# Kernel optimization log

Hardware: AMD Instinct MI355X
Metric: run time of the kernel (lower is better)

## Reference

```python
import jax, jax.numpy as jnp
import numpy as np

EPS = 1e-06

def rotate_half(x):
    d = x.shape[-1] // 2
    return jnp.concatenate([-x[..., d:], x[..., :d]], axis=-1)

def rmsnorm(x, w):
    rms = jnp.sqrt(jnp.mean(x * x, axis=-1, keepdims=True) + EPS)
    return (x / rms) * w

def setup_inputs() -> dict:
    key = jax.random.key(0)
    ks = jax.random.split(key, 12)
    H, Hq, Hkv, Dh, S, C = 2048, 16, 8, 128, 1, 16384
    sc = 0.02
    return {
        "hidden_states": jax.random.normal(ks[0], (1, 1, S, H), jnp.float32),
        "cos": jax.random.uniform(ks[1], (1, 1, S, Dh), jnp.float32),
        "sin": jax.random.uniform(ks[2], (1, 1, S, Dh), jnp.float32),
        "attention_mask": jnp.zeros((1, 1, S, C + S), jnp.float32),
        "k_cache": jax.random.normal(ks[3], (Hkv, Dh, C), jnp.float32),
        "v_cache": jax.random.normal(ks[4], (Hkv, C, Dh), jnp.float32),
        "Wq": jax.random.normal(ks[5], (Hq, Dh, H), jnp.float32) * sc,
        "Wk": jax.random.normal(ks[6], (Hkv, Dh, H), jnp.float32) * sc,
        "Wv": jax.random.normal(ks[7], (Hkv, Dh, H), jnp.float32) * sc,
        "Wo": jax.random.normal(ks[8], (H, Hq * Dh), jnp.float32) * sc,
        "q_norm_w": jnp.ones((Dh,), jnp.float32),
        "k_norm_w": jnp.ones((Dh,), jnp.float32),
    }

def reference(hidden_states, cos, sin, attention_mask, k_cache, v_cache, Wq, Wk, Wv, Wo, q_norm_w, k_norm_w):
    S = hidden_states.shape[2]
    Hq, Dh = Wq.shape[0], Wq.shape[1]
    Hkv = Wk.shape[0]
    g = Hq // Hkv
    x = hidden_states.reshape(S, -1)                      # [S, H]
    # per-head 1x1 conv == per-head linear; batched as einsum
    q = rmsnorm(jnp.einsum('sh,qdh->qsd', x, Wq), q_norm_w)   # [Hq, S, Dh]
    k = rmsnorm(jnp.einsum('sh,kdh->ksd', x, Wk), k_norm_w)   # [Hkv, S, Dh]
    v = jnp.einsum('sh,kdh->ksd', x, Wv)                      # [Hkv, S, Dh]
    c = cos.reshape(S, Dh)
    s = sin.reshape(S, Dh)
    q = q * c + rotate_half(q) * s
    k_new = k * c + rotate_half(k) * s
    # KV cache concat: k stored transposed [Hkv, Dh, C]
    k_full = jnp.concatenate([k_cache, jnp.swapaxes(k_new, 1, 2)], axis=2)  # [Hkv, Dh, C+S]
    v_full = jnp.concatenate([v_cache, v], axis=1)                          # [Hkv, C+S, Dh]
    kf = jnp.repeat(k_full, g, axis=0)                    # GQA expand -> [Hq, Dh, C+S]
    vf = jnp.repeat(v_full, g, axis=0)                    # [Hq, C+S, Dh]
    scaling = Dh ** -0.5
    scores = jnp.einsum('qsd,qdc->qsc', q, kf) * scaling + attention_mask.reshape(1, S, -1)
    probs = jax.nn.softmax(scores, axis=-1)
    out = jnp.einsum('qsc,qcd->qsd', probs, vf)           # [Hq, S, Dh]
    out = jnp.transpose(out, (1, 0, 2)).reshape(S, Hq * Dh)  # head-major last dim
    attn = out @ Wo.T                                     # o_proj 1x1 conv
    return attn.reshape(1, 1, S, -1), k_new, v
```

## Files before the change

kernel.cpp:

```cpp
#include <hip/hip_runtime.h>
#include <math.h>
#include <stddef.h>

#define HQ   16
#define HKV  8
#define DH   128
#define HID  2048
#define CC   16384
#define NCH  128
#define CHUNK 128


__global__ void k_qkv(const float* __restrict__ x,
                      const float* __restrict__ Wq,
                      const float* __restrict__ Wk,
                      const float* __restrict__ Wv,
                      float* __restrict__ raw,
                      float* __restrict__ out){
  int wave = threadIdx.x >> 6, lane = threadIdx.x & 63;
  int e = blockIdx.x * 4 + wave;
  const float* W;
  if (e < 2048)      W = Wq + (size_t)e * HID;
  else if (e < 3072) W = Wk + (size_t)(e - 2048) * HID;
  else               W = Wv + (size_t)(e - 3072) * HID;
  float4 wb[8], xb[8];
  #pragma unroll
  for (int j = 0; j < 8; ++j) wb[j] = *(const float4*)(W + (j * 64 + lane) * 4);
  #pragma unroll
  for (int j = 0; j < 8; ++j) xb[j] = *(const float4*)(x + (j * 64 + lane) * 4);
  float acc = 0.f;
  #pragma unroll
  for (int j = 0; j < 8; ++j)
    acc += wb[j].x*xb[j].x + wb[j].y*xb[j].y + wb[j].z*xb[j].z + wb[j].w*xb[j].w;
  #pragma unroll
  for (int off = 32; off; off >>= 1) acc += __shfl_down(acc, off, 64);
  if (lane == 0){
    raw[e] = acc;
    if (e >= 3072) out[e] = acc;
  }
}

__global__ void k_normrope(const float* __restrict__ raw,
                           const float* __restrict__ cosb,
                           const float* __restrict__ sinb,
                           const float* __restrict__ qw,
                           const float* __restrict__ kw,
                           float* __restrict__ qf,
                           float* __restrict__ kf,
                           float* __restrict__ out){
  __shared__ float lds[DH];
  __shared__ float wsum[2];
  int b = blockIdx.x, t = threadIdx.x;
  bool isq = (b < 16);
  int h = isq ? b : b - 16;
  float val = isq ? raw[h * DH + t] : raw[2048 + h * DH + t];
  float ss = val * val;
  #pragma unroll
  for (int off = 32; off; off >>= 1) ss += __shfl_down(ss, off, 64);
  if ((t & 63) == 0) wsum[t >> 6] = ss;
  __syncthreads();
  float rms = sqrtf((wsum[0] + wsum[1]) / 128.f + 1e-6f);
  float w = isq ? qw[t] : kw[t];
  float normed = val / rms * w;
  lds[t] = normed;
  __syncthreads();
  float rot = (t < 64) ? -lds[t + 64] : lds[t - 64];
  float res = normed * cosb[t] + rot * sinb[t];
  if (isq) qf[h * DH + t] = res;
  else { kf[h * DH + t] = res; out[2048 + h * DH + t] = res; }
}

__global__ __launch_bounds__(256, 4) void k_flash(
    const float* __restrict__ qf,
    const float* __restrict__ kcache,
    const float* __restrict__ vcache,
    const float* __restrict__ mask,
    float* __restrict__ opart,
    float2* __restrict__ ml){
  __shared__ float q_s[2][DH];
  __shared__ float sc_part[8][2][CHUNK];
  __shared__ float p_s[2][CHUNK];
  __shared__ float part[2][8][DH];
  __shared__ float red[8];
  int kv = blockIdx.x >> 7, ch = blockIdx.x & 127;
  int c0 = ch << 7;
  int t = threadIdx.x;
  q_s[t >> 7][t & 127] = qf[(kv * 2 + (t >> 7)) * DH + (t & 127)];
  __syncthreads();
  const float scale = 0.08838834764831845f;

  {
    int dg = t >> 5, ln = t & 31;
    const float* kp = kcache + (size_t)kv * DH * CC + (size_t)(dg * 16) * CC + (c0 + ln * 4);
    float4 k0[8], k1[8];
    #pragma unroll
    for (int j = 0; j < 8; ++j) k0[j] = *(const float4*)(kp + (size_t)j * CC);
    #pragma unroll
    for (int j = 0; j < 8; ++j) k1[j] = *(const float4*)(kp + (size_t)(j + 8) * CC);
    float a00 = 0.f, a01 = 0.f, a02 = 0.f, a03 = 0.f;
    float a10 = 0.f, a11 = 0.f, a12 = 0.f, a13 = 0.f;
    #pragma unroll
    for (int j = 0; j < 8; ++j){
      float q0 = q_s[0][dg * 16 + j], q1 = q_s[1][dg * 16 + j];
      a00 += q0 * k0[j].x; a01 += q0 * k0[j].y; a02 += q0 * k0[j].z; a03 += q0 * k0[j].w;
      a10 += q1 * k0[j].x; a11 += q1 * k0[j].y; a12 += q1 * k0[j].z; a13 += q1 * k0[j].w;
    }
    #pragma unroll
    for (int j = 0; j < 8; ++j){
      float q0 = q_s[0][dg * 16 + 8 + j], q1 = q_s[1][dg * 16 + 8 + j];
      a00 += q0 * k1[j].x; a01 += q0 * k1[j].y; a02 += q0 * k1[j].z; a03 += q0 * k1[j].w;
      a10 += q1 * k1[j].x; a11 += q1 * k1[j].y; a12 += q1 * k1[j].z; a13 += q1 * k1[j].w;
    }
    *(float4*)&sc_part[dg][0][ln * 4] = make_float4(a00, a01, a02, a03);
    *(float4*)&sc_part[dg][1][ln * 4] = make_float4(a10, a11, a12, a13);
  }
  __syncthreads();

  int sl = t >> 5, d4 = (t & 31) * 4;
  const float* vbase = vcache + (size_t)kv * CC * DH + (size_t)c0 * DH + d4;
  float4 vv0[8];
  #pragma unroll
  for (int j = 0; j < 8; ++j)
    vv0[j] = *(const float4*)(vbase + (size_t)(j * 8 + sl) * DH);

  int h = t >> 7, pos = t & 127;
  float s;
  {
    float acc = 0.f;
    #pragma unroll
    for (int dg = 0; dg < 8; ++dg) acc += sc_part[dg][h][pos];
    s = acc * scale + mask[c0 + pos];
  }
  int wv = t >> 6;
  float lm = s;
  #pragma unroll
  for (int off = 32; off; off >>= 1) lm = fmaxf(lm, __shfl_down(lm, off, 64));
  if ((t & 63) == 0) red[wv] = lm;
  __syncthreads();
  float m = fmaxf(red[h * 2], red[h * 2 + 1]);
  float p = __expf(s - m);
  p_s[h][pos] = p;
  float lsum = p;
  #pragma unroll
  for (int off = 32; off; off >>= 1) lsum += __shfl_down(lsum, off, 64);
  if ((t & 63) == 0) red[4 + wv] = lsum;
  __syncthreads();
  if ((t & 127) == 0){
    float l = red[4 + h * 2] + red[5 + h * 2];
    ml[(size_t)(kv * 2 + h) * NCH + ch] = make_float2(m, l);
  }

  {
    float4 vv1[8];
    #pragma unroll
    for (int j = 0; j < 8; ++j)
      vv1[j] = *(const float4*)(vbase + (size_t)((j + 8) * 8 + sl) * DH);
    float4 a0 = make_float4(0.f, 0.f, 0.f, 0.f);
    float4 a1 = make_float4(0.f, 0.f, 0.f, 0.f);
    #pragma unroll
    for (int j = 0; j < 8; ++j){
      int off = j * 8 + sl;
      float pp0 = p_s[0][off], pp1 = p_s[1][off];
      a0.x += pp0 * vv0[j].x; a0.y += pp0 * vv0[j].y; a0.z += pp0 * vv0[j].z; a0.w += pp0 * vv0[j].w;
      a1.x += pp1 * vv0[j].x; a1.y += pp1 * vv0[j].y; a1.z += pp1 * vv0[j].z; a1.w += pp1 * vv0[j].w;
    }
    #pragma unroll
    for (int j = 0; j < 8; ++j){
      int off = (j + 8) * 8 + sl;
      float pp0 = p_s[0][off], pp1 = p_s[1][off];
      a0.x += pp0 * vv1[j].x; a0.y += pp0 * vv1[j].y; a0.z += pp0 * vv1[j].z; a0.w += pp0 * vv1[j].w;
      a1.x += pp1 * vv1[j].x; a1.y += pp1 * vv1[j].y; a1.z += pp1 * vv1[j].z; a1.w += pp1 * vv1[j].w;
    }
    *(float4*)&part[0][sl][d4] = a0;
    *(float4*)&part[1][sl][d4] = a1;
  }
  __syncthreads();
  {
    int hh = t >> 7, d = t & 127;
    float o = 0.f;
    #pragma unroll
    for (int ss = 0; ss < 8; ++ss) o += part[hh][ss][d];
    int qh = kv * 2 + hh;
    opart[((size_t)qh * NCH + ch) * DH + d] = o;
  }
}

__global__ void k_combine(const float* __restrict__ opart,
                          const float2* __restrict__ ml,
                          const float* __restrict__ qf,
                          const float* __restrict__ kf,
                          const float* __restrict__ vnew,
                          const float* __restrict__ mask,
                          float* __restrict__ attn_in){
  __shared__ float osum[4][DH];
  __shared__ float Ls[4];
  __shared__ float redm[8];
  __shared__ float redq[2];
  int qh = blockIdx.x, t = threadIdx.x;
  int g = t >> 7, d = t & 127;
  int kv = qh >> 1;
  const float2* mlrow = ml + (size_t)qh * NCH;
  float mm = mlrow[t & 127].x;
  #pragma unroll
  for (int off = 32; off; off >>= 1) mm = fmaxf(mm, __shfl_down(mm, off, 64));
  if ((t & 63) == 0) redm[t >> 6] = mm;
  __syncthreads();
  float M = fmaxf(redm[0], redm[1]);
  float o = 0.f, L = 0.f;
  int ch0 = g * 32;
  #pragma unroll 4
  for (int i = 0; i < 32; ++i){
    float2 m2 = mlrow[ch0 + i];
    float w = __expf(m2.x - M);
    L += m2.y * w;
    o += w * opart[((size_t)qh * NCH + ch0 + i) * DH + d];
  }
  osum[g][d] = o;
  if (d == 0) Ls[g] = L;
  if (t < DH){
    float sum = qf[qh * DH + t] * kf[kv * DH + t];
    #pragma unroll
    for (int off = 32; off; off >>= 1) sum += __shfl_down(sum, off, 64);
    if ((t & 63) == 0) redq[t >> 6] = sum;
  }
  __syncthreads();
  if (t < DH){
    float s_new = (redq[0] + redq[1]) * 0.08838834764831845f + mask[CC];
    float pn = __expf(s_new - M);
    float Lf = Ls[0] + Ls[1] + Ls[2] + Ls[3] + pn;
    float of = osum[0][t] + osum[1][t] + osum[2][t] + osum[3][t]
             + pn * vnew[kv * DH + t];
    attn_in[qh * DH + t] = of / Lf;
  }
}

__global__ void k_oproj(const float* __restrict__ attn_in,
                        const float* __restrict__ Wo,
                        float* __restrict__ out){
  int wave = threadIdx.x >> 6, lane = threadIdx.x & 63;
  int e = blockIdx.x * 4 + wave;
  const float* W = Wo + (size_t)e * HID;
  float4 wb[8], xb[8];
  #pragma unroll
  for (int j = 0; j < 8; ++j) wb[j] = *(const float4*)(W + (j * 64 + lane) * 4);
  #pragma unroll
  for (int j = 0; j < 8; ++j) xb[j] = *(const float4*)(attn_in + (j * 64 + lane) * 4);
  float acc = 0.f;
  #pragma unroll
  for (int j = 0; j < 8; ++j)
    acc += wb[j].x*xb[j].x + wb[j].y*xb[j].y + wb[j].z*xb[j].z + wb[j].w*xb[j].w;
  #pragma unroll
  for (int off = 32; off; off >>= 1) acc += __shfl_down(acc, off, 64);
  if (lane == 0) out[e] = acc;
}

extern "C" void kernel_launch(void* const* d_in, const int* in_sizes, int n_in,
                              void* d_out, int out_size, void* d_ws, size_t ws_size,
                              hipStream_t stream){
  const float* x    = (const float*)d_in[0];
  const float* cosb = (const float*)d_in[1];
  const float* sinb = (const float*)d_in[2];
  const float* mask = (const float*)d_in[3];
  const float* kc   = (const float*)d_in[4];
  const float* vc   = (const float*)d_in[5];
  const float* Wq   = (const float*)d_in[6];
  const float* Wk   = (const float*)d_in[7];
  const float* Wv   = (const float*)d_in[8];
  const float* Wo   = (const float*)d_in[9];
  const float* qw   = (const float*)d_in[10];
  const float* kw   = (const float*)d_in[11];
  float* out = (float*)d_out;
  float* ws = (float*)d_ws;
  float* raw     = ws;
  float* qf      = ws + 4096;
  float* kf      = ws + 6144;
  float* opart   = ws + 8192;
  float2* ML     = (float2*)(ws + 270336);
  float* attn_in = ws + 274432;

  k_qkv     <<<1024, 256, 0, stream>>>(x, Wq, Wk, Wv, raw, out);
  k_normrope<<<24,   128, 0, stream>>>(raw, cosb, sinb, qw, kw, qf, kf, out);
  k_flash   <<<HKV * NCH, 256, 0, stream>>>(qf, kc, vc, mask, opart, ML);
  k_combine <<<HQ, 512, 0, stream>>>(opart, ML, qf, kf, raw + 3072, mask, attn_in);
  k_oproj   <<<512, 256, 0, stream>>>(attn_in, Wo, out);
}
```

Baseline: 216.3 us.

## Use larger KV chunks with 512-thread flash-decode blocks

The split-K attention kernel now processes 512 cache positions per block with 512 threads instead of 128 positions with 256 threads. That cuts the number of partial results from 128 to 32 per head, shrinking the combine kernel's work and the workspace. K and V loads are issued in batches with scheduling barriers to keep loads grouped ahead of the FMAs, and the same barriers are added to the QKV and output projection GEMVs. The trade-off is fewer blocks (one per CU) and fewer resident waves per CU, which may reduce how much memory latency can be hidden in this bandwidth-bound kernel.

```diff
diff --git a/kernel.cpp b/kernel.cpp
--- a/kernel.cpp
+++ b/kernel.cpp
@@ -7,8 +7,8 @@
 #define DH   128
 #define HID  2048
 #define CC   16384
-#define NCH  128
-#define CHUNK 128
+#define NCH  32
+#define CHUNK 512
 
 
 __global__ void k_qkv(const float* __restrict__ x,
@@ -28,6 +28,7 @@
   for (int j = 0; j < 8; ++j) wb[j] = *(const float4*)(W + (j * 64 + lane) * 4);
   #pragma unroll
   for (int j = 0; j < 8; ++j) xb[j] = *(const float4*)(x + (j * 64 + lane) * 4);
+  __builtin_amdgcn_sched_barrier(0);
   float acc = 0.f;
   #pragma unroll
   for (int j = 0; j < 8; ++j)
@@ -70,7 +71,7 @@
   else { kf[h * DH + t] = res; out[2048 + h * DH + t] = res; }
 }
 
-__global__ __launch_bounds__(256, 4) void k_flash(
+__global__ __launch_bounds__(512) void k_flash(
     const float* __restrict__ qf,
     const float* __restrict__ kcache,
     const float* __restrict__ vcache,
@@ -80,106 +81,133 @@
   __shared__ float q_s[2][DH];
   __shared__ float sc_part[8][2][CHUNK];
   __shared__ float p_s[2][CHUNK];
-  __shared__ float part[2][8][DH];
-  __shared__ float red[8];
-  int kv = blockIdx.x >> 7, ch = blockIdx.x & 127;
-  int c0 = ch << 7;
+  __shared__ float part[2][16][DH];
+  __shared__ float red[32];
+  int kv = blockIdx.x >> 5, ch = blockIdx.x & 31;
+  int c0 = ch << 9;
   int t = threadIdx.x;
-  q_s[t >> 7][t & 127] = qf[(kv * 2 + (t >> 7)) * DH + (t & 127)];
+  if (t < 256) q_s[t >> 7][t & 127] = qf[(kv * 2 + (t >> 7)) * DH + (t & 127)];
   __syncthreads();
   const float scale = 0.08838834764831845f;
 
   {
-    int dg = t >> 5, ln = t & 31;
-    const float* kp = kcache + (size_t)kv * DH * CC + (size_t)(dg * 16) * CC + (c0 + ln * 4);
-    float4 k0[8], k1[8];
-    #pragma unroll
-    for (int j = 0; j < 8; ++j) k0[j] = *(const float4*)(kp + (size_t)j * CC);
-    #pragma unroll
-    for (int j = 0; j < 8; ++j) k1[j] = *(const float4*)(kp + (size_t)(j + 8) * CC);
-    float a00 = 0.f, a01 = 0.f, a02 = 0.f, a03 = 0.f;
-    float a10 = 0.f, a11 = 0.f, a12 = 0.f, a13 = 0.f;
-    #pragma unroll
-    for (int j = 0; j < 8; ++j){
-      float q0 = q_s[0][dg * 16 + j], q1 = q_s[1][dg * 16 + j];
-      a00 += q0 * k0[j].x; a01 += q0 * k0[j].y; a02 += q0 * k0[j].z; a03 += q0 * k0[j].w;
-      a10 += q1 * k0[j].x; a11 += q1 * k0[j].y; a12 += q1 * k0[j].z; a13 += q1 * k0[j].w;
+    int dg = t >> 6, ln = t & 63;
+    const float* kp = kcache + (size_t)kv * DH * CC + (size_t)(dg * 16) * CC + c0 + ln * 4;
+    float qr0[16], qr1[16];
+    #pragma unroll
+    for (int i = 0; i < 16; ++i){
+      qr0[i] = q_s[0][dg * 16 + i];
+      qr1[i] = q_s[1][dg * 16 + i];
     }
     #pragma unroll
-    for (int j = 0; j < 8; ++j){
-      float q0 = q_s[0][dg * 16 + 8 + j], q1 = q_s[1][dg * 16 + 8 + j];
-      a00 += q0 * k1[j].x; a01 += q0 * k1[j].y; a02 += q0 * k1[j].z; a03 += q0 * k1[j].w;
-      a10 += q1 * k1[j].x; a11 += q1 * k1[j].y; a12 += q1 * k1[j].z; a13 += q1 * k1[j].w;
+    for (int half = 0; half < 2; ++half){
+      const float* kph = kp + half * 256;
+      float4 kb[8], kc2[8];
+      #pragma unroll
+      for (int j = 0; j < 8; ++j) kb[j]  = *(const float4*)(kph + (size_t)j * CC);
+      #pragma unroll
+      for (int j = 0; j < 8; ++j) kc2[j] = *(const float4*)(kph + (size_t)(j + 8) * CC);
+      __builtin_amdgcn_sched_barrier(0);
+      float a00 = 0.f, a01 = 0.f, a02 = 0.f, a03 = 0.f;
+      float a10 = 0.f, a11 = 0.f, a12 = 0.f, a13 = 0.f;
+      #pragma unroll
+      for (int j = 0; j < 8; ++j){
+        a00 += qr0[j] * kb[j].x;  a01 += qr0[j] * kb[j].y;
+        a02 += qr0[j] * kb[j].z;  a03 += qr0[j] * kb[j].w;
+        a10 += qr1[j] * kb[j].x;  a11 += qr1[j] * kb[j].y;
+        a12 += qr1[j] * kb[j].z;  a13 += qr1[j] * kb[j].w;
+      }
+      #pragma unroll
+      for (int j = 0; j < 8; ++j){
+        a00 += qr0[8 + j] * kc2[j].x;  a01 += qr0[8 + j] * kc2[j].y;
+        a02 += qr0[8 + j] * kc2[j].z;  a03 += qr0[8 + j] * kc2[j].w;
+        a10 += qr1[8 + j] * kc2[j].x;  a11 += qr1[8 + j] * kc2[j].y;
+        a12 += qr1[8 + j] * kc2[j].z;  a13 += qr1[8 + j] * kc2[j].w;
+      }
+      *(float4*)&sc_part[dg][0][half * 256 + ln * 4] = make_float4(a00, a01, a02, a03);
+      *(float4*)&sc_part[dg][1][half * 256 + ln * 4] = make_float4(a10, a11, a12, a13);
     }
-    *(float4*)&sc_part[dg][0][ln * 4] = make_float4(a00, a01, a02, a03);
-    *(float4*)&sc_part[dg][1][ln * 4] = make_float4(a10, a11, a12, a13);
-  }
-  __syncthreads();
-
-  int sl = t >> 5, d4 = (t & 31) * 4;
-  const float* vbase = vcache + (size_t)kv * CC * DH + (size_t)c0 * DH + d4;
-  float4 vv0[8];
-  #pragma unroll
-  for (int j = 0; j < 8; ++j)
-    vv0[j] = *(const float4*)(vbase + (size_t)(j * 8 + sl) * DH);
-
-  int h = t >> 7, pos = t & 127;
-  float s;
+  }
+  __syncthreads();
+
+  int wv = t >> 6;
+  float s0, s1;
   {
-    float acc = 0.f;
-    #pragma unroll
-    for (int dg = 0; dg < 8; ++dg) acc += sc_part[dg][h][pos];
-    s = acc * scale + mask[c0 + pos];
-  }
-  int wv = t >> 6;
-  float lm = s;
-  #pragma unroll
-  for (int off = 32; off; off >>= 1) lm = fmaxf(lm, __shfl_down(lm, off, 64));
-  if ((t & 63) == 0) red[wv] = lm;
-  __syncthreads();
-  float m = fmaxf(red[h * 2], red[h * 2 + 1]);
-  float p = __expf(s - m);
-  p_s[h][pos] = p;
-  float lsum = p;
-  #pragma unroll
-  for (int off = 32; off; off >>= 1) lsum += __shfl_down(lsum, off, 64);
-  if ((t & 63) == 0) red[4 + wv] = lsum;
-  __syncthreads();
-  if ((t & 127) == 0){
-    float l = red[4 + h * 2] + red[5 + h * 2];
-    ml[(size_t)(kv * 2 + h) * NCH + ch] = make_float2(m, l);
+    float acc0 = 0.f, acc1 = 0.f;
+    #pragma unroll
+    for (int dg = 0; dg < 8; ++dg){
+      acc0 += sc_part[dg][0][t];
+      acc1 += sc_part[dg][1][t];
+    }
+    float mk = mask[c0 + t];
+    s0 = acc0 * scale + mk;
+    s1 = acc1 * scale + mk;
+  }
+  float lm0 = s0, lm1 = s1;
+  #pragma unroll
+  for (int off = 32; off; off >>= 1){
+    lm0 = fmaxf(lm0, __shfl_down(lm0, off, 64));
+    lm1 = fmaxf(lm1, __shfl_down(lm1, off, 64));
+  }
+  if ((t & 63) == 0){ red[wv] = lm0; red[8 + wv] = lm1; }
+  __syncthreads();
+  float m0 = red[0], m1 = red[8];
+  #pragma unroll
+  for (int i = 1; i < 8; ++i){
+    m0 = fmaxf(m0, red[i]);
+    m1 = fmaxf(m1, red[8 + i]);
+  }
+  float p0 = __expf(s0 - m0);
+  float p1 = __expf(s1 - m1);
+  p_s[0][t] = p0;
+  p_s[1][t] = p1;
+  float ls0 = p0, ls1 = p1;
+  #pragma unroll
+  for (int off = 32; off; off >>= 1){
+    ls0 += __shfl_down(ls0, off, 64);
+    ls1 += __shfl_down(ls1, off, 64);
+  }
+  if ((t & 63) == 0){ red[16 + wv] = ls0; red[24 + wv] = ls1; }
+  __syncthreads();
+  if (t == 0){
+    float l0 = 0.f, l1 = 0.f;
+    #pragma unroll
+    for (int i = 0; i < 8; ++i){ l0 += red[16 + i]; l1 += red[24 + i]; }
+    ml[(size_t)(kv * 2)     * NCH + ch] = make_float2(m0, l0);
+    ml[(size_t)(kv * 2 + 1) * NCH + ch] = make_float2(m1, l1);
   }
 
   {
-    float4 vv1[8];
-    #pragma unroll
-    for (int j = 0; j < 8; ++j)
-      vv1[j] = *(const float4*)(vbase + (size_t)((j + 8) * 8 + sl) * DH);
+    int sl = t >> 5, d4 = (t & 31) * 4;
+    const float* vbase = vcache + (size_t)kv * CC * DH + (size_t)c0 * DH + d4;
     float4 a0 = make_float4(0.f, 0.f, 0.f, 0.f);
     float4 a1 = make_float4(0.f, 0.f, 0.f, 0.f);
     #pragma unroll
-    for (int j = 0; j < 8; ++j){
-      int off = j * 8 + sl;
-      float pp0 = p_s[0][off], pp1 = p_s[1][off];
-      a0.x += pp0 * vv0[j].x; a0.y += pp0 * vv0[j].y; a0.z += pp0 * vv0[j].z; a0.w += pp0 * vv0[j].w;
-      a1.x += pp1 * vv0[j].x; a1.y += pp1 * vv0[j].y; a1.z += pp1 * vv0[j].z; a1.w += pp1 * vv0[j].w;
-    }
-    #pragma unroll
-    for (int j = 0; j < 8; ++j){
-      int off = (j + 8) * 8 + sl;
-      float pp0 = p_s[0][off], pp1 = p_s[1][off];
-      a0.x += pp0 * vv1[j].x; a0.y += pp0 * vv1[j].y; a0.z += pp0 * vv1[j].z; a0.w += pp0 * vv1[j].w;
-      a1.x += pp1 * vv1[j].x; a1.y += pp1 * vv1[j].y; a1.z += pp1 * vv1[j].z; a1.w += pp1 * vv1[j].w;
+    for (int ib = 0; ib < 4; ++ib){
+      float4 vv[8];
+      #pragma unroll
+      for (int j = 0; j < 8; ++j){
+        int off = (ib * 8 + j) * 16 + sl;
+        vv[j] = *(const float4*)(vbase + (size_t)off * DH);
+      }
+      __builtin_amdgcn_sched_barrier(0);
+      #pragma unroll
+      for (int j = 0; j < 8; ++j){
+        int off = (ib * 8 + j) * 16 + sl;
+        float pp0 = p_s[0][off], pp1 = p_s[1][off];
+        a0.x += pp0 * vv[j].x; a0.y += pp0 * vv[j].y; a0.z += pp0 * vv[j].z; a0.w += pp0 * vv[j].w;
+        a1.x += pp1 * vv[j].x; a1.y += pp1 * vv[j].y; a1.z += pp1 * vv[j].z; a1.w += pp1 * vv[j].w;
+      }
     }
     *(float4*)&part[0][sl][d4] = a0;
     *(float4*)&part[1][sl][d4] = a1;
   }
   __syncthreads();
-  {
+  if (t < 256){
     int hh = t >> 7, d = t & 127;
     float o = 0.f;
     #pragma unroll
-    for (int ss = 0; ss < 8; ++ss) o += part[hh][ss][d];
+    for (int ss = 0; ss < 16; ++ss) o += part[hh][ss][d];
     int qh = kv * 2 + hh;
     opart[((size_t)qh * NCH + ch) * DH + d] = o;
   }
@@ -200,16 +228,16 @@
   int g = t >> 7, d = t & 127;
   int kv = qh >> 1;
   const float2* mlrow = ml + (size_t)qh * NCH;
-  float mm = mlrow[t & 127].x;
+  float mm = mlrow[t & 31].x;
   #pragma unroll
   for (int off = 32; off; off >>= 1) mm = fmaxf(mm, __shfl_down(mm, off, 64));
   if ((t & 63) == 0) redm[t >> 6] = mm;
   __syncthreads();
   float M = fmaxf(redm[0], redm[1]);
   float o = 0.f, L = 0.f;
-  int ch0 = g * 32;
-  #pragma unroll 4
-  for (int i = 0; i < 32; ++i){
+  int ch0 = g * 8;
+  #pragma unroll
+  for (int i = 0; i < 8; ++i){
     float2 m2 = mlrow[ch0 + i];
     float w = __expf(m2.x - M);
     L += m2.y * w;
@@ -245,6 +273,7 @@
   for (int j = 0; j < 8; ++j) wb[j] = *(const float4*)(W + (j * 64 + lane) * 4);
   #pragma unroll
   for (int j = 0; j < 8; ++j) xb[j] = *(const float4*)(attn_in + (j * 64 + lane) * 4);
+  __builtin_amdgcn_sched_barrier(0);
   float acc = 0.f;
   #pragma unroll
   for (int j = 0; j < 8; ++j)
@@ -275,12 +304,12 @@
   float* qf      = ws + 4096;
   float* kf      = ws + 6144;
   float* opart   = ws + 8192;
-  float2* ML     = (float2*)(ws + 270336);
-  float* attn_in = ws + 274432;
+  float2* ML     = (float2*)(ws + 73728);
+  float* attn_in = ws + 74752;
 
   k_qkv     <<<1024, 256, 0, stream>>>(x, Wq, Wk, Wv, raw, out);
   k_normrope<<<24,   128, 0, stream>>>(raw, cosb, sinb, qw, kw, qf, kf, out);
-  k_flash   <<<HKV * NCH, 256, 0, stream>>>(qf, kc, vc, mask, opart, ML);
+  k_flash   <<<HKV * NCH, 512, 0, stream>>>(qf, kc, vc, mask, opart, ML);
   k_combine <<<HQ, 512, 0, stream>>>(opart, ML, qf, kf, raw + 3072, mask, attn_in);
   k_oproj   <<<512, 256, 0, stream>>>(attn_in, Wo, out);
 }
```

Result: no change. 212.9 us (-1.6%).
